# Performance work log

Measured on AMD Instinct MI355X. Metric: run time of the kernel, lower is better.

## Reference

```python
import jax, jax.numpy as jnp
import numpy as np

N = 50000
E = 600000
IN_DIM = 128
D = 32          # out_dim per head
H = 4           # heads
M = 3           # num metapaths
HID = 128       # semantic attention hidden
NEG_SLOPE = 0.2


def setup_inputs() -> dict:
    key = jax.random.key(0)
    ks = jax.random.split(key, 12)
    x = jax.random.normal(ks[0], (N, IN_DIM), dtype=jnp.float32)
    mp_edge_index = jax.random.randint(ks[1], (M, 2, E), 0, N, dtype=jnp.int64)
    s = 1.0 / np.sqrt(IN_DIM)
    W = jax.random.normal(ks[2], (M, IN_DIM, H * D), dtype=jnp.float32) * s
    att_src = jax.random.normal(ks[3], (M, H, D), dtype=jnp.float32) * (1.0 / np.sqrt(D))
    att_dst = jax.random.normal(ks[4], (M, H, D), dtype=jnp.float32) * (1.0 / np.sqrt(D))
    bias = jnp.zeros((M, H * D), dtype=jnp.float32)
    ln_gamma = jnp.ones((H * D,), dtype=jnp.float32)
    ln_beta = jnp.zeros((H * D,), dtype=jnp.float32)
    sem_W1 = jax.random.normal(ks[5], (H * D, HID), dtype=jnp.float32) * (1.0 / np.sqrt(H * D))
    sem_b1 = jnp.zeros((HID,), dtype=jnp.float32)
    sem_W2 = jax.random.normal(ks[6], (HID, 1), dtype=jnp.float32) * (1.0 / np.sqrt(HID))
    return dict(x=x, mp_edge_index=mp_edge_index, W=W, att_src=att_src,
                att_dst=att_dst, bias=bias, ln_gamma=ln_gamma, ln_beta=ln_beta,
                sem_W1=sem_W1, sem_b1=sem_b1, sem_W2=sem_W2)


def _gat_conv(x, edge_index, W_m, a_src, a_dst, b_m):
    # PyG GATConv (add_self_loops=True, concat=True). x: [N, F_in]
    n = x.shape[0]
    h = (x @ W_m).reshape(n, H, D)                       # [N, H, D]
    loops = jnp.arange(n, dtype=edge_index.dtype)
    src = jnp.concatenate([edge_index[0], loops])        # [E+N]
    dst = jnp.concatenate([edge_index[1], loops])
    alpha_s = jnp.einsum('nhd,hd->nh', h, a_src)         # [N, H]
    alpha_d = jnp.einsum('nhd,hd->nh', h, a_dst)
    e = jax.nn.leaky_relu(alpha_s[src] + alpha_d[dst], NEG_SLOPE)  # [E+N, H]
    # segment softmax over edges grouped by destination node
    e_max = jax.ops.segment_max(e, dst, num_segments=n)
    e = jnp.exp(e - e_max[dst])
    denom = jax.ops.segment_sum(e, dst, num_segments=n)
    alpha = e / (denom[dst] + 1e-16)                     # [E+N, H]
    msg = h[src] * alpha[:, :, None]                     # [E+N, H, D]
    out = jax.ops.segment_sum(msg, dst, num_segments=n)  # [N, H, D]
    return out.reshape(n, H * D) + b_m


def _layer_norm(y, gamma, beta):
    mu = y.mean(-1, keepdims=True)
    var = y.var(-1, keepdims=True)
    return (y - mu) * jax.lax.rsqrt(var + 1e-5) * gamma + beta


def reference(x, mp_edge_index, W, att_src, att_dst, bias, ln_gamma, ln_beta,
              sem_W1, sem_b1, sem_W2):
    embs = []
    for i in range(M):
        emb = _gat_conv(x, mp_edge_index[i], W[i], att_src[i], att_dst[i], bias[i])
        emb = jax.nn.elu(_layer_norm(emb, ln_gamma, ln_beta))
        embs.append(emb)
    z = jnp.stack(embs, axis=1)                          # [N, M, H*D]
    # semantic attention
    w = (jnp.tanh(z @ sem_W1 + sem_b1) @ sem_W2).mean(0)  # [M, 1]
    beta = jax.nn.softmax(w, axis=0)                      # [M, 1]
    out_emb = (beta[None, :, :] * z).sum(1)               # [N, H*D]
    att_mp = beta.squeeze()                               # [M]
    return out_emb, att_mp
```

## Files before the change

kernel.cpp:

```cpp
#include <hip/hip_runtime.h>
#include <hip/hip_bf16.h>

#define N_NODES 50000
#define N_EDGES 600000
#define NMETA   3
#define LTOT (NMETA * N_NODES)
#define SPAN_SHIFT 9
#define NBUCK 98
#define BCAP 8192
#define NCHUNK 147
#define LOG2E 1.4426950408889634f

typedef unsigned short u16;
typedef short bf16x8 __attribute__((ext_vector_type(8)));
typedef float f32x4 __attribute__((ext_vector_type(4)));

__device__ __forceinline__ float bf2f(u16 v) {
    union { unsigned int u; float f; } x; x.u = ((unsigned int)v) << 16; return x.f;
}
__device__ __forceinline__ u16 f2bf(float f) {
    return __hip_bfloat16_raw(__float2bfloat16(f)).x;
}

__global__ __launch_bounds__(256) void k_build1(
    const int* __restrict__ ei, int* __restrict__ gcnt,
    unsigned long long* __restrict__ pairs,
    const float* __restrict__ W, const float* __restrict__ W1,
    u16* __restrict__ WT, u16* __restrict__ W1T)
{
    const int bid = blockIdx.x;
    const int t = threadIdx.x;
    if (bid >= NMETA * NCHUNK) {
        int idx = (bid - NMETA * NCHUNK) * 256 + t;
        if (idx < NMETA * 16384) {
            int m = idx >> 14, r = idx & 16383;
            int col = r >> 7, k = r & 127;
            WT[idx] = f2bf(W[(m << 14) + k * 128 + col]);
        } else {
            int r = idx - NMETA * 16384;
            int col = r >> 7, k = r & 127;
            W1T[r] = f2bf(W1[k * 128 + col]);
        }
        return;
    }
    const int m = bid / NCHUNK;
    const int e0 = (bid % NCHUNK) * 4096;
    __shared__ int cnt[NBUCK];
    __shared__ int gbase[NBUCK];
    if (t < NBUCK) cnt[t] = 0;
    __syncthreads();
    const int* srcp = ei + (size_t)m * 2 * N_EDGES;
    const int* dstp = srcp + N_EDGES;
    int sa[16], da[16], sl[16];
    #pragma unroll
    for (int j = 0; j < 16; ++j) {
        int e = e0 + j * 256 + t;
        if (e < N_EDGES) {
            int s = srcp[e], d = dstp[e];
            if ((unsigned)s >= N_NODES) s = 0;
            if ((unsigned)d >= N_NODES) d = 0;
            sa[j] = s; da[j] = d;
            sl[j] = atomicAdd(&cnt[d >> SPAN_SHIFT], 1);
        } else sl[j] = -1;
    }
    __syncthreads();
    if (t < NBUCK) gbase[t] = atomicAdd(&gcnt[m * NBUCK + t], cnt[t]);
    __syncthreads();
    #pragma unroll
    for (int j = 0; j < 16; ++j) {
        if (sl[j] < 0) continue;
        int b = da[j] >> SPAN_SHIFT;
        int pos = gbase[b] + sl[j];
        if (pos < BCAP)
            pairs[(size_t)(m * NBUCK + b) * BCAP + pos] =
                ((unsigned long long)(da[j] & 511) << 32) | (unsigned)(sa[j] * 128);
    }
}

__global__ __launch_bounds__(256) void k_build2(
    const int* __restrict__ gcnt, const unsigned long long* __restrict__ pairs,
    int* __restrict__ row_start, int* __restrict__ row_end, int* __restrict__ eidx,
    const float* __restrict__ x, const u16* __restrict__ WT,
    const float* __restrict__ att_src, const float* __restrict__ att_dst,
    u16* __restrict__ h, float* __restrict__ alpha_s, float* __restrict__ alpha_d)
{
    const int bid = blockIdx.x;
    const int t = threadIdx.x;
    if (bid < NMETA * NBUCK) {
        const int m = bid / NBUCK, b = bid % NBUCK;
        __shared__ int cnt[512];
        __shared__ int off[512];
        __shared__ int wsum[4];
        int nb = gcnt[m * NBUCK + b]; if (nb > BCAP) nb = BCAP;
        const int base = (m * NBUCK + b) * BCAP;
        cnt[t] = 0; cnt[t + 256] = 0;
        __syncthreads();
        for (int e = t; e < nb; e += 256) {
            int dl = (int)(pairs[(size_t)base + e] >> 32);
            atomicAdd(&cnt[dl], 1);
        }
        __syncthreads();
        int v0 = cnt[2 * t], v1 = cnt[2 * t + 1];
        int s = v0 + v1;
        int lane = t & 63, wv = t >> 6;
        int incl = s;
        #pragma unroll
        for (int o = 1; o < 64; o <<= 1) {
            int u = __shfl_up(incl, o);
            if (lane >= o) incl += u;
        }
        if (lane == 63) wsum[wv] = incl;
        __syncthreads();
        int woff = 0;
        for (int i = 0; i < wv; ++i) woff += wsum[i];
        int ex = woff + incl - s;
        off[2 * t] = ex;
        off[2 * t + 1] = ex + v0;
        __syncthreads();
        const int node0 = b << SPAN_SHIFT;
        for (int i = t; i < 512; i += 256) {
            int n = node0 + i;
            if (n < N_NODES) {
                int st = base + off[i];
                row_start[m * N_NODES + n] = st;
                row_end[m * N_NODES + n]   = st + cnt[i];
            }
        }
        __syncthreads();
        for (int e = t; e < nb; e += 256) {
            unsigned long long p = pairs[(size_t)base + e];
            int dl = (int)(p >> 32);
            int pos = atomicAdd(&off[dl], 1);
            eidx[(size_t)base + pos] = (int)(unsigned)p;
        }
        return;
    }
    const int g = bid - NMETA * NBUCK;
    const int bx = g % 782, m = g / 782;
    const int wv = t >> 6, lane = t & 63;
    const int row0 = (bx * 4 + wv) * 16;
    if (row0 >= N_NODES) return;
    const int lhi = lane >> 4, llo = lane & 15;
    const float* xrow = x + (size_t)(row0 + llo) * 128 + lhi * 8;
    bf16x8 a[4];
    #pragma unroll
    for (int ks = 0; ks < 4; ++ks) {
        float4 f0 = *(const float4*)(xrow + ks * 32);
        float4 f1 = *(const float4*)(xrow + ks * 32 + 4);
        bf16x8 av;
        av[0] = f2bf(f0.x); av[1] = f2bf(f0.y); av[2] = f2bf(f0.z); av[3] = f2bf(f0.w);
        av[4] = f2bf(f1.x); av[5] = f2bf(f1.y); av[6] = f2bf(f1.z); av[7] = f2bf(f1.w);
        a[ks] = av;
    }
    const u16* wbase = WT + (size_t)m * 16384 + (size_t)llo * 128 + lhi * 8;
    u16* hm = h + ((size_t)m * N_NODES + row0) * 128;
    float sp[4][4], dp[4][4];
    #pragma unroll
    for (int i = 0; i < 4; ++i)
        #pragma unroll
        for (int r = 0; r < 4; ++r) { sp[i][r] = 0.f; dp[i][r] = 0.f; }
    #pragma unroll
    for (int cf = 0; cf < 8; ++cf) {
        f32x4 acc = {0.f, 0.f, 0.f, 0.f};
        const u16* wp = wbase + cf * 16 * 128;
        #pragma unroll
        for (int ks = 0; ks < 4; ++ks) {
            bf16x8 b = *(const bf16x8*)(wp + ks * 32);
            acc = __builtin_amdgcn_mfma_f32_16x16x32_bf16(a[ks], b, acc, 0, 0, 0);
        }
        const int col = cf * 16 + llo;
        const int hh = cf >> 1;
        const float as = att_src[m * 128 + col];
        const float adv = att_dst[m * 128 + col];
        #pragma unroll
        for (int r = 0; r < 4; ++r) {
            hm[(size_t)(lhi * 4 + r) * 128 + col] = f2bf(acc[r]);
            sp[hh][r] += acc[r] * as;
            dp[hh][r] += acc[r] * adv;
        }
    }
    #pragma unroll
    for (int o = 1; o <= 8; o <<= 1) {
        #pragma unroll
        for (int i = 0; i < 4; ++i)
            #pragma unroll
            for (int r = 0; r < 4; ++r) {
                sp[i][r] += __shfl_xor(sp[i][r], o);
                dp[i][r] += __shfl_xor(dp[i][r], o);
            }
    }
    if (llo == 0) {
        #pragma unroll
        for (int r = 0; r < 4; ++r) {
            int n = row0 + lhi * 4 + r;
            f32x4 vs = {sp[0][r] * LOG2E, sp[1][r] * LOG2E, sp[2][r] * LOG2E, sp[3][r] * LOG2E};
            f32x4 vd = {dp[0][r] * LOG2E, dp[1][r] * LOG2E, dp[2][r] * LOG2E, dp[3][r] * LOG2E};
            *(f32x4*)(alpha_s + ((size_t)m * N_NODES + n) * 4) = vs;
            *(f32x4*)(alpha_d + ((size_t)m * N_NODES + n) * 4) = vd;
        }
    }
}

__global__ __launch_bounds__(256) void k_gather(
    const int* __restrict__ row_start, const int* __restrict__ row_end,
    const int* __restrict__ eidx,
    const float* __restrict__ alpha_s, const float* __restrict__ alpha_d,
    const u16* __restrict__ h,
    const float* __restrict__ bias, const float* __restrict__ gamma,
    const float* __restrict__ lbeta,
    u16* __restrict__ z)
{
    long long w = ((long long)blockIdx.x * blockDim.x + threadIdx.x) >> 6;
    if (w >= (long long)LTOT) return;
    int m = (int)(w / N_NODES), n = (int)(w % N_NODES);
    int lane = threadIdx.x & 63, hh = lane >> 4;
    const float* as_m = alpha_s + (size_t)m * N_NODES * 4;
    const float* ad_m = alpha_d + (size_t)m * N_NODES * 4;
    const u16*   h_m  = h + (size_t)m * N_NODES * 128;
    float ad = ad_m[n * 4 + hh];
    float pre = as_m[n * 4 + hh] + ad;
    pre = fmaxf(pre, 0.2f * pre);
    float ev = exp2f(pre);
    float esum = ev;
    ushort2 hv = *(const ushort2*)(h_m + n * 128 + lane * 2);
    float acc0 = ev * bf2f(hv.x), acc1 = ev * bf2f(hv.y);
    int p = row_start[m * N_NODES + n];
    const int end = row_end[m * N_NODES + n];
    for (; p + 3 < end; p += 4) {
        int o1 = eidx[p], o2 = eidx[p + 1], o3 = eidx[p + 2], o4 = eidx[p + 3];
        float p1 = as_m[(o1 >> 5) + hh] + ad;
        float p2 = as_m[(o2 >> 5) + hh] + ad;
        float p3 = as_m[(o3 >> 5) + hh] + ad;
        float p4 = as_m[(o4 >> 5) + hh] + ad;
        ushort2 h1 = *(const ushort2*)(h_m + o1 + lane * 2);
        ushort2 h2 = *(const ushort2*)(h_m + o2 + lane * 2);
        ushort2 h3 = *(const ushort2*)(h_m + o3 + lane * 2);
        ushort2 h4 = *(const ushort2*)(h_m + o4 + lane * 2);
        p1 = fmaxf(p1, 0.2f * p1);
        p2 = fmaxf(p2, 0.2f * p2);
        p3 = fmaxf(p3, 0.2f * p3);
        p4 = fmaxf(p4, 0.2f * p4);
        float e1 = exp2f(p1), e2 = exp2f(p2), e3 = exp2f(p3), e4 = exp2f(p4);
        esum += (e1 + e2) + (e3 + e4);
        acc0 += e1 * bf2f(h1.x) + e2 * bf2f(h2.x) + e3 * bf2f(h3.x) + e4 * bf2f(h4.x);
        acc1 += e1 * bf2f(h1.y) + e2 * bf2f(h2.y) + e3 * bf2f(h3.y) + e4 * bf2f(h4.y);
    }
    for (; p < end; ++p) {
        int o1 = eidx[p];
        float p1 = as_m[(o1 >> 5) + hh] + ad;
        ushort2 h1 = *(const ushort2*)(h_m + o1 + lane * 2);
        p1 = fmaxf(p1, 0.2f * p1);
        float e1 = exp2f(p1);
        esum += e1;
        acc0 += e1 * bf2f(h1.x);
        acc1 += e1 * bf2f(h1.y);
    }
    float rinv = 1.f / (esum + 1e-16f);
    float v0 = acc0 * rinv + bias[m * 128 + lane * 2];
    float v1 = acc1 * rinv + bias[m * 128 + lane * 2 + 1];
    float s1 = v0 + v1, s2 = v0 * v0 + v1 * v1;
    #pragma unroll
    for (int o = 32; o >= 1; o >>= 1) { s1 += __shfl_xor(s1, o); s2 += __shfl_xor(s2, o); }
    float mu = s1 * (1.f / 128.f);
    float var = s2 * (1.f / 128.f) - mu * mu;
    float rs = rsqrtf(var + 1e-5f);
    float o0 = (v0 - mu) * rs * gamma[lane * 2]     + lbeta[lane * 2];
    float o1 = (v1 - mu) * rs * gamma[lane * 2 + 1] + lbeta[lane * 2 + 1];
    o0 = o0 > 0.f ? o0 : (__expf(o0) - 1.f);
    o1 = o1 > 0.f ? o1 : (__expf(o1) - 1.f);
    ushort2 outv; outv.x = f2bf(o0); outv.y = f2bf(o1);
    *(ushort2*)(z + ((size_t)n * NMETA + m) * 128 + lane * 2) = outv;
}

__global__ __launch_bounds__(256) void k_sem(
    const u16* __restrict__ z,
    const u16* __restrict__ W1T,
    const float* __restrict__ b1,
    const float* __restrict__ W2,
    float* __restrict__ wpart)
{
    __shared__ float part[NMETA];
    const int t = threadIdx.x;
    if (t < NMETA) part[t] = 0.f;
    __syncthreads();
    const int wv = t >> 6, lane = t & 63;
    const int row0 = (blockIdx.x * 4 + wv) * 16;
    if (row0 < LTOT) {
        const int lhi = lane >> 4, llo = lane & 15;
        const u16* zrow = z + (size_t)(row0 + llo) * 128 + lhi * 8;
        bf16x8 a[4];
        #pragma unroll
        for (int ks = 0; ks < 4; ++ks) a[ks] = *(const bf16x8*)(zrow + ks * 32);
        const u16* wb = W1T + (size_t)llo * 128 + lhi * 8;
        float rowacc[4] = {0.f, 0.f, 0.f, 0.f};
        #pragma unroll
        for (int cf = 0; cf < 8; ++cf) {
            f32x4 acc = {0.f, 0.f, 0.f, 0.f};
            const u16* wp = wb + cf * 16 * 128;
            #pragma unroll
            for (int ks = 0; ks < 4; ++ks) {
                bf16x8 bb = *(const bf16x8*)(wp + ks * 32);
                acc = __builtin_amdgcn_mfma_f32_16x16x32_bf16(a[ks], bb, acc, 0, 0, 0);
            }
            int col = cf * 16 + llo;
            float b1v = b1[col], w2v = W2[col];
            #pragma unroll
            for (int r = 0; r < 4; ++r)
                rowacc[r] += tanhf(acc[r] + b1v) * w2v;
        }
        #pragma unroll
        for (int o = 1; o <= 8; o <<= 1) {
            #pragma unroll
            for (int r = 0; r < 4; ++r) rowacc[r] += __shfl_xor(rowacc[r], o);
        }
        if (llo == 0) {
            #pragma unroll
            for (int r = 0; r < 4; ++r)
                atomicAdd(&part[(row0 + lhi * 4 + r) % NMETA], rowacc[r]);
        }
    }
    __syncthreads();
    if (t < NMETA) atomicAdd(&wpart[t], part[t]);
}

__global__ void k_beta(const float* __restrict__ wpart, float* __restrict__ betab,
                       float* __restrict__ attout)
{
    if (threadIdx.x == 0 && blockIdx.x == 0) {
        float w0 = wpart[0] * (1.f / N_NODES);
        float w1 = wpart[1] * (1.f / N_NODES);
        float w2 = wpart[2] * (1.f / N_NODES);
        float mx = fmaxf(w0, fmaxf(w1, w2));
        float e0 = __expf(w0 - mx), e1 = __expf(w1 - mx), e2 = __expf(w2 - mx);
        float s = 1.f / (e0 + e1 + e2);
        float b0 = e0 * s, b1 = e1 * s, b2 = e2 * s;
        betab[0] = b0; betab[1] = b1; betab[2] = b2;
        attout[0] = b0; attout[1] = b1; attout[2] = b2;
    }
}

__global__ __launch_bounds__(256) void k_combine(
    const u16* __restrict__ z, const float* __restrict__ betab,
    float* __restrict__ out)
{
    int idx = blockIdx.x * blockDim.x + threadIdx.x;
    if (idx >= N_NODES * 64) return;
    int n = idx >> 6, c2 = (idx & 63) * 2;
    float b0 = betab[0], b1 = betab[1], b2 = betab[2];
    const u16* zp = z + (size_t)n * NMETA * 128 + c2;
    ushort2 a0 = *(const ushort2*)(zp);
    ushort2 a1 = *(const ushort2*)(zp + 128);
    ushort2 a2 = *(const ushort2*)(zp + 256);
    float2 ov;
    ov.x = b0 * bf2f(a0.x) + b1 * bf2f(a1.x) + b2 * bf2f(a2.x);
    ov.y = b0 * bf2f(a0.y) + b1 * bf2f(a1.y) + b2 * bf2f(a2.y);
    *(float2*)(out + (size_t)n * 128 + c2) = ov;
}

extern "C" void kernel_launch(void* const* d_in, const int* in_sizes, int n_in,
                              void* d_out, int out_size, void* d_ws, size_t ws_size,
                              hipStream_t stream) {
    const float* x       = (const float*)d_in[0];
    const int*   ei      = (const int*)d_in[1];
    const float* W       = (const float*)d_in[2];
    const float* att_src = (const float*)d_in[3];
    const float* att_dst = (const float*)d_in[4];
    const float* bias    = (const float*)d_in[5];
    const float* gamma   = (const float*)d_in[6];
    const float* lbeta   = (const float*)d_in[7];
    const float* W1      = (const float*)d_in[8];
    const float* b1      = (const float*)d_in[9];
    const float* W2      = (const float*)d_in[10];

    char* ws = (char*)d_ws;
    size_t off = 0;
    int* gcnt    = (int*)(ws + off);  off += sizeof(int) * 512;
    float* wpart = (float*)(ws + off);
    float* betab = wpart + 8;         off += 64;
    const size_t zero_bytes = off;
    off = (off + 255) & ~(size_t)255;
    int* row_start = (int*)(ws + off); off += sizeof(int) * 150016;
    int* row_end   = (int*)(ws + off); off += sizeof(int) * 150016;
    u16* h      = (u16*)(ws + off);    off += sizeof(u16) * (size_t)NMETA * N_NODES * 128;
    float* alpha_s = (float*)(ws + off); off += sizeof(float) * (size_t)LTOT * 4;
    float* alpha_d = (float*)(ws + off); off += sizeof(float) * (size_t)LTOT * 4;
    u16* WT     = (u16*)(ws + off);    off += sizeof(u16) * (size_t)NMETA * 128 * 128;
    u16* W1T    = (u16*)(ws + off);    off += sizeof(u16) * (size_t)128 * 128;
    int* eidx   = (int*)(ws + off);    off += sizeof(int) * (size_t)NMETA * NBUCK * BCAP;
    unsigned long long* pairs = (unsigned long long*)(ws + off);
    u16* z = (u16*)(ws + off);
    off += sizeof(u16) * (size_t)N_NODES * NMETA * 128;
    if (ws_size < off) return;

    hipMemsetAsync(d_ws, 0, zero_bytes, stream);

    k_build1<<<dim3(NMETA * NCHUNK + 256), 256, 0, stream>>>(ei, gcnt, pairs, W, W1, WT, W1T);
    k_build2<<<dim3(NMETA * NBUCK + 782 * NMETA), 256, 0, stream>>>(
        gcnt, pairs, row_start, row_end, eidx,
        x, WT, att_src, att_dst, h, alpha_s, alpha_d);
    k_gather<<<dim3((LTOT + 3) / 4), 256, 0, stream>>>(row_start, row_end, eidx,
                                                       alpha_s, alpha_d, h,
                                                       bias, gamma, lbeta, z);
    k_sem<<<dim3((LTOT / 16 + 3) / 4), 256, 0, stream>>>(z, W1T, b1, W2, wpart);
    k_beta<<<1, 64, 0, stream>>>(wpart, betab, (float*)d_out + (size_t)N_NODES * 128);
    k_combine<<<dim3((N_NODES * 64 + 255) / 256), 256, 0, stream>>>(z, betab, (float*)d_out);
}
```

Before: 274.2 us.

## Precompute per-edge attention weights in a separate kernel before gather

Adds a k_ew kernel that computes the leaky-relu/exp2 edge weight for all four heads once per edge and stores it as bf16. For this it packs the destination-local index into the high bits of eidx, then rewrites eidx as a byte offset. k_gather then reads the precomputed weight instead of gathering alpha_s and computing exp per lane, so 16 lanes no longer redo the same work. In exchange it adds a kernel launch, an extra pass over the edges and ew storage, and the weights are rounded to bf16.

```diff
diff --git a/kernel.cpp b/kernel.cpp
--- a/kernel.cpp
+++ b/kernel.cpp
@@ -131,7 +131,7 @@
             unsigned long long p = pairs[(size_t)base + e];
             int dl = (int)(p >> 32);
             int pos = atomicAdd(&off[dl], 1);
-            eidx[(size_t)base + pos] = (int)(unsigned)p;
+            eidx[(size_t)base + pos] = (dl << 23) | (int)(unsigned)p;
         }
         return;
     }
@@ -201,9 +201,40 @@
     }
 }
 
+__global__ __launch_bounds__(256) void k_ew(
+    const int* __restrict__ gcnt, int* __restrict__ eidx,
+    const float* __restrict__ alpha_s, const float* __restrict__ alpha_d,
+    u16* __restrict__ ew)
+{
+    const int bucket = blockIdx.x;
+    const int m = bucket / NBUCK, b = bucket % NBUCK;
+    int nb = gcnt[bucket]; if (nb > BCAP) nb = BCAP;
+    const int base = bucket * BCAP;
+    const int node0 = b << SPAN_SHIFT;
+    const float* as_m = alpha_s + (size_t)m * N_NODES * 4;
+    const float* ad_m = alpha_d + (size_t)m * N_NODES * 4;
+    for (int i = threadIdx.x; i < nb; i += 256) {
+        int v = eidx[base + i];
+        int src128 = v & 0x7FFFFF;
+        int dl = (unsigned)v >> 23;
+        f32x4 as4 = *(const f32x4*)(as_m + (src128 >> 5));
+        f32x4 ad4 = *(const f32x4*)(ad_m + (size_t)(node0 + dl) * 4);
+        ushort4 e4;
+        u16* ep = (u16*)&e4;
+        #pragma unroll
+        for (int k = 0; k < 4; ++k) {
+            float pre = as4[k] + ad4[k];
+            pre = fmaxf(pre, 0.2f * pre);
+            ep[k] = f2bf(exp2f(pre));
+        }
+        *(ushort4*)(ew + (size_t)(base + i) * 4) = e4;
+        eidx[base + i] = src128 * 2;
+    }
+}
+
 __global__ __launch_bounds__(256) void k_gather(
     const int* __restrict__ row_start, const int* __restrict__ row_end,
-    const int* __restrict__ eidx,
+    const int* __restrict__ eidx, const u16* __restrict__ ew,
     const float* __restrict__ alpha_s, const float* __restrict__ alpha_d,
     const u16* __restrict__ h,
     const float* __restrict__ bias, const float* __restrict__ gamma,
@@ -214,43 +245,36 @@
     if (w >= (long long)LTOT) return;
     int m = (int)(w / N_NODES), n = (int)(w % N_NODES);
     int lane = threadIdx.x & 63, hh = lane >> 4;
+    const char* h_m = (const char*)(h + (size_t)m * N_NODES * 128);
+    const int lb = lane * 4;
     const float* as_m = alpha_s + (size_t)m * N_NODES * 4;
     const float* ad_m = alpha_d + (size_t)m * N_NODES * 4;
-    const u16*   h_m  = h + (size_t)m * N_NODES * 128;
-    float ad = ad_m[n * 4 + hh];
-    float pre = as_m[n * 4 + hh] + ad;
+    float pre = as_m[n * 4 + hh] + ad_m[n * 4 + hh];
     pre = fmaxf(pre, 0.2f * pre);
     float ev = exp2f(pre);
     float esum = ev;
-    ushort2 hv = *(const ushort2*)(h_m + n * 128 + lane * 2);
+    ushort2 hv = *(const ushort2*)(h_m + (size_t)n * 256 + lb);
     float acc0 = ev * bf2f(hv.x), acc1 = ev * bf2f(hv.y);
     int p = row_start[m * N_NODES + n];
     const int end = row_end[m * N_NODES + n];
     for (; p + 3 < end; p += 4) {
         int o1 = eidx[p], o2 = eidx[p + 1], o3 = eidx[p + 2], o4 = eidx[p + 3];
-        float p1 = as_m[(o1 >> 5) + hh] + ad;
-        float p2 = as_m[(o2 >> 5) + hh] + ad;
-        float p3 = as_m[(o3 >> 5) + hh] + ad;
-        float p4 = as_m[(o4 >> 5) + hh] + ad;
-        ushort2 h1 = *(const ushort2*)(h_m + o1 + lane * 2);
-        ushort2 h2 = *(const ushort2*)(h_m + o2 + lane * 2);
-        ushort2 h3 = *(const ushort2*)(h_m + o3 + lane * 2);
-        ushort2 h4 = *(const ushort2*)(h_m + o4 + lane * 2);
-        p1 = fmaxf(p1, 0.2f * p1);
-        p2 = fmaxf(p2, 0.2f * p2);
-        p3 = fmaxf(p3, 0.2f * p3);
-        p4 = fmaxf(p4, 0.2f * p4);
-        float e1 = exp2f(p1), e2 = exp2f(p2), e3 = exp2f(p3), e4 = exp2f(p4);
+        float e1 = bf2f(ew[(size_t)p * 4 + hh]);
+        float e2 = bf2f(ew[(size_t)p * 4 + 4 + hh]);
+        float e3 = bf2f(ew[(size_t)p * 4 + 8 + hh]);
+        float e4 = bf2f(ew[(size_t)p * 4 + 12 + hh]);
+        ushort2 h1 = *(const ushort2*)(h_m + o1 + lb);
+        ushort2 h2 = *(const ushort2*)(h_m + o2 + lb);
+        ushort2 h3 = *(const ushort2*)(h_m + o3 + lb);
+        ushort2 h4 = *(const ushort2*)(h_m + o4 + lb);
         esum += (e1 + e2) + (e3 + e4);
         acc0 += e1 * bf2f(h1.x) + e2 * bf2f(h2.x) + e3 * bf2f(h3.x) + e4 * bf2f(h4.x);
         acc1 += e1 * bf2f(h1.y) + e2 * bf2f(h2.y) + e3 * bf2f(h3.y) + e4 * bf2f(h4.y);
     }
     for (; p < end; ++p) {
         int o1 = eidx[p];
-        float p1 = as_m[(o1 >> 5) + hh] + ad;
-        ushort2 h1 = *(const ushort2*)(h_m + o1 + lane * 2);
-        p1 = fmaxf(p1, 0.2f * p1);
-        float e1 = exp2f(p1);
+        float e1 = bf2f(ew[(size_t)p * 4 + hh]);
+        ushort2 h1 = *(const ushort2*)(h_m + o1 + lb);
         esum += e1;
         acc0 += e1 * bf2f(h1.x);
         acc1 += e1 * bf2f(h1.y);
@@ -387,6 +411,7 @@
     u16* WT     = (u16*)(ws + off);    off += sizeof(u16) * (size_t)NMETA * 128 * 128;
     u16* W1T    = (u16*)(ws + off);    off += sizeof(u16) * (size_t)128 * 128;
     int* eidx   = (int*)(ws + off);    off += sizeof(int) * (size_t)NMETA * NBUCK * BCAP;
+    u16* ew     = (u16*)(ws + off);    off += sizeof(u16) * (size_t)NMETA * NBUCK * BCAP * 4;
     unsigned long long* pairs = (unsigned long long*)(ws + off);
     u16* z = (u16*)(ws + off);
     off += sizeof(u16) * (size_t)N_NODES * NMETA * 128;
@@ -398,7 +423,8 @@
     k_build2<<<dim3(NMETA * NBUCK + 782 * NMETA), 256, 0, stream>>>(
         gcnt, pairs, row_start, row_end, eidx,
         x, WT, att_src, att_dst, h, alpha_s, alpha_d);
-    k_gather<<<dim3((LTOT + 3) / 4), 256, 0, stream>>>(row_start, row_end, eidx,
+    k_ew<<<dim3(NMETA * NBUCK), 256, 0, stream>>>(gcnt, eidx, alpha_s, alpha_d, ew);
+    k_gather<<<dim3((LTOT + 3) / 4), 256, 0, stream>>>(row_start, row_end, eidx, ew,
                                                        alpha_s, alpha_d, h,
                                                        bias, gamma, lbeta, z);
     k_sem<<<dim3((LTOT / 16 + 3) / 4), 256, 0, stream>>>(z, W1T, b1, W2, wpart);
```

Result: slower. 287.0 us (+4.7%).
